# Performance work log

Hardware: AMD Instinct MI355X
Metric: run time of the kernel (lower is better)

Reference implementation:

```python
import jax, jax.numpy as jnp
import numpy as np

D_MODEL = 1024
NUM_HEADS = 16
HEAD_DIM = D_MODEL // NUM_HEADS


def setup_inputs() -> dict:
    key = jax.random.key(0)
    ks = jax.random.split(key, 9)
    B, S = 2, 2048
    s = 1.0 / np.sqrt(D_MODEL)
    return {
        "x": jax.random.normal(ks[0], (B, S, D_MODEL), dtype=jnp.float32),
        "Wq": jax.random.normal(ks[1], (D_MODEL, D_MODEL), dtype=jnp.float32) * s,
        "bq": jnp.zeros((D_MODEL,), dtype=jnp.float32),
        "Wk": jax.random.normal(ks[2], (D_MODEL, D_MODEL), dtype=jnp.float32) * s,
        "bk": jnp.zeros((D_MODEL,), dtype=jnp.float32),
        "Wv": jax.random.normal(ks[3], (D_MODEL, D_MODEL), dtype=jnp.float32) * s,
        "bv": jnp.zeros((D_MODEL,), dtype=jnp.float32),
        "Wo": jax.random.normal(ks[4], (D_MODEL, D_MODEL), dtype=jnp.float32) * s,
        "bo": jnp.zeros((D_MODEL,), dtype=jnp.float32),
    }


def reference(x, Wq, bq, Wk, bk, Wv, bv, Wo, bo):
    B, S, _ = x.shape
    # linear projections then split heads: [B, S, D] -> [B, H, S, hd]
    def split_heads(t):
        return t.reshape(B, S, NUM_HEADS, HEAD_DIM).transpose(0, 2, 1, 3)
    q = split_heads(x @ Wq + bq)
    k = split_heads(x @ Wk + bk)
    v = split_heads(x @ Wv + bv)
    # scores: [B, H, S, S]
    scores = jnp.einsum('bhqd,bhkd->bhqk', q, k) / jnp.sqrt(
        jnp.asarray(HEAD_DIM, dtype=x.dtype))
    attn = jax.nn.softmax(scores, axis=-1)
    # dropout is identity in eval mode
    out = jnp.einsum('bhqk,bhkd->bhqd', attn, v)
    out = out.transpose(0, 2, 1, 3).reshape(B, S, D_MODEL)
    return out @ Wo + bo
```

## Files before the change

### kernel.cpp

```cpp
#include <hip/hip_runtime.h>

#define D_MODEL 1024
#define NHEAD 16
#define HD 64
#define BATCH 2
#define SEQ 2048

typedef unsigned short u16;
typedef unsigned int u32;
typedef __bf16 bf16x8 __attribute__((ext_vector_type(8)));
typedef unsigned short u16x8 __attribute__((ext_vector_type(8)));
typedef short s16x4 __attribute__((ext_vector_type(4)));
typedef float f32x4 __attribute__((ext_vector_type(4)));

#if defined(__has_builtin)
#if __has_builtin(__builtin_amdgcn_exp2f)
#define EXP2(x) __builtin_amdgcn_exp2f(x)
#else
#define EXP2(x) exp2f(x)
#endif
#else
#define EXP2(x) exp2f(x)
#endif

static __device__ __forceinline__ u16 f2bf(float f) {
    union { float f; unsigned u; } v; v.f = f;
    unsigned u = v.u;
    u += 0x7fffu + ((u >> 16) & 1u);
    return (u16)(u >> 16);
}

static __device__ __forceinline__ void gld_lds16(const void* g, void* l) {
    __builtin_amdgcn_global_load_lds(
        (const __attribute__((address_space(1))) void*)g,
        (__attribute__((address_space(3))) void*)l, 16, 0, 0);
}

static __device__ __forceinline__ bf16x8 pack_bf8(f32x4 a, f32x4 b) {
    union { float f; unsigned u; } a0, a1, a2, a3, b0, b1, b2, b3;
    a0.f = a[0]; a1.f = a[1]; a2.f = a[2]; a3.f = a[3];
    b0.f = b[0]; b1.f = b[1]; b2.f = b[2]; b3.f = b[3];
    union { unsigned u[4]; bf16x8 v; } r;
    r.u[0] = __builtin_amdgcn_perm(a1.u, a0.u, 0x07060302u);
    r.u[1] = __builtin_amdgcn_perm(a3.u, a2.u, 0x07060302u);
    r.u[2] = __builtin_amdgcn_perm(b1.u, b0.u, 0x07060302u);
    r.u[3] = __builtin_amdgcn_perm(b3.u, b2.u, 0x07060302u);
    return r.v;
}

__global__ __launch_bounds__(256) void k_convert(const float* __restrict__ x,
                                                 const float* __restrict__ wq,
                                                 const float* __restrict__ wk,
                                                 const float* __restrict__ wv,
                                                 const float* __restrict__ wo,
                                                 u16* __restrict__ xb,
                                                 u16* __restrict__ wt) {
    int z = blockIdx.z;
    if (z == 0) {
        int base = (blockIdx.y * 32 + blockIdx.x) * 256 + threadIdx.x;
#pragma unroll
        for (int p = 0; p < 4; p++) {
            int i = base + p * 262144;
            float4 v = ((const float4*)x)[i];
            ushort4 o = make_ushort4(f2bf(v.x), f2bf(v.y), f2bf(v.z), f2bf(v.w));
            ((ushort4*)xb)[i] = o;
        }
        return;
    }
    __shared__ u16 t[32][33];
    const float* W = z == 1 ? wq : z == 2 ? wk : z == 3 ? wv : wo;
    u16* dst = wt + (size_t)(z - 1) * (D_MODEL * D_MODEL);
    int tx = threadIdx.x & 31, ty = threadIdx.x >> 5;
    int n0 = blockIdx.x * 32, k0 = blockIdx.y * 32;
#pragma unroll
    for (int i = 0; i < 4; i++)
        t[ty + i * 8][tx] = f2bf(W[(size_t)(k0 + ty + i * 8) * D_MODEL + n0 + tx]);
    __syncthreads();
#pragma unroll
    for (int i = 0; i < 4; i++)
        dst[(size_t)(n0 + ty + i * 8) * D_MODEL + k0 + tx] = t[tx][ty + i * 8];
}

__global__ __launch_bounds__(256) void k_gemm(const u16* __restrict__ A,
                                              const u16* __restrict__ WtBase,
                                              const float* __restrict__ b0,
                                              const float* __restrict__ b1,
                                              const float* __restrict__ b2,
                                              u16* __restrict__ oq, u16* __restrict__ ok,
                                              u16* __restrict__ ov) {
    __shared__ u16 lA[2 * 128 * 32];
    __shared__ u16 lB[2 * 128 * 32];
    int tid = threadIdx.x, w = tid >> 6, l = tid & 63, lr = l & 15, lq = l >> 4;
    int z = blockIdx.z;
    const u16* Wt = WtBase + (size_t)z * (D_MODEL * D_MODEL);
    const float* bias = z == 0 ? b0 : z == 1 ? b1 : b2;
    float scale = (z == 0) ? (0.125f * 1.44269504088896340736f) : 1.0f;
    int m0 = blockIdx.y * 128, n0 = blockIdx.x * 128;
    int wm = (w >> 1) * 64, wn = (w & 1) * 64;
    f32x4 acc[4][4];
#pragma unroll
    for (int mi = 0; mi < 4; mi++)
#pragma unroll
        for (int ni = 0; ni < 4; ni++) acc[mi][ni] = (f32x4){0.f, 0.f, 0.f, 0.f};

    int ra = tid >> 2, ca = (tid & 3) * 8;
    const u16* Aba = A + (size_t)(m0 + ra) * D_MODEL + ca;
    const u16* Abb = A + (size_t)(m0 + 64 + ra) * D_MODEL + ca;
    const u16* Bba = Wt + (size_t)(n0 + ra) * D_MODEL + ca;
    const u16* Bbb = Wt + (size_t)(n0 + 64 + ra) * D_MODEL + ca;

    auto stage = [&](int kk, int buf) {
        gld_lds16(Aba + kk, &lA[buf * 4096 + w * 512]);
        gld_lds16(Abb + kk, &lA[buf * 4096 + 2048 + w * 512]);
        gld_lds16(Bba + kk, &lB[buf * 4096 + w * 512]);
        gld_lds16(Bbb + kk, &lB[buf * 4096 + 2048 + w * 512]);
    };

    stage(0, 0);
    __syncthreads();
    int cur = 0;
    for (int t = 0; t < 32; ++t) {
        if (t + 1 < 32) stage((t + 1) * 32, cur ^ 1);
        bf16x8 af[4], bf[4];
#pragma unroll
        for (int mi = 0; mi < 4; mi++)
            af[mi] = *(const bf16x8*)&lA[cur * 4096 + (wm + mi * 16 + lr) * 32 + lq * 8];
#pragma unroll
        for (int ni = 0; ni < 4; ni++)
            bf[ni] = *(const bf16x8*)&lB[cur * 4096 + (wn + ni * 16 + lr) * 32 + lq * 8];
        __builtin_amdgcn_s_setprio(1);
#pragma unroll
        for (int mi = 0; mi < 4; mi++)
#pragma unroll
            for (int ni = 0; ni < 4; ni++)
                acc[mi][ni] = __builtin_amdgcn_mfma_f32_16x16x32_bf16(
                    af[mi], bf[ni], acc[mi][ni], 0, 0, 0);
        __builtin_amdgcn_s_setprio(0);
        __syncthreads();
        cur ^= 1;
    }
#pragma unroll
    for (int mi = 0; mi < 4; mi++) {
#pragma unroll
        for (int ni = 0; ni < 4; ni++) {
            int col = n0 + wn + ni * 16 + lr;
            float bval = bias[col];
            int row0 = m0 + wm + mi * 16 + lq * 4;
            if (z == 2) {
                int b = row0 >> 11, s = row0 & 2047;
                int h = col >> 6, dd = col & 63;
                ushort4 pk;
                pk.x = f2bf(acc[mi][ni][0] + bval);
                pk.y = f2bf(acc[mi][ni][1] + bval);
                pk.z = f2bf(acc[mi][ni][2] + bval);
                pk.w = f2bf(acc[mi][ni][3] + bval);
                *(ushort4*)&ov[((size_t)(b * NHEAD + h) * HD + dd) * SEQ + s] = pk;
            } else {
#pragma unroll
                for (int r = 0; r < 4; r++) {
                    int row = row0 + r;
                    float val = (acc[mi][ni][r] + bval) * scale;
                    u16* op = z == 0 ? oq : ok;
                    int b = row >> 11, s = row & 2047, h = col >> 6, d = col & 63;
                    op[(((size_t)(b * NHEAD + h)) * SEQ + s) * HD + d] = f2bf(val);
                }
            }
        }
    }
}

__global__ __launch_bounds__(256) void k_gout(const u16* __restrict__ A,
                                              const u16* __restrict__ Wt,
                                              const float* __restrict__ bias,
                                              float* __restrict__ outf) {
    __shared__ u16 lA[2 * 64 * 32];
    __shared__ u16 lB[2 * 64 * 32];
    int tid = threadIdx.x, w = tid >> 6, l = tid & 63, lr = l & 15, lq = l >> 4;
    int m0 = blockIdx.y * 64, n0 = blockIdx.x * 64;
    int wm = (w >> 1) * 32, wn = (w & 1) * 32;
    f32x4 acc[2][2];
#pragma unroll
    for (int mi = 0; mi < 2; mi++)
#pragma unroll
        for (int ni = 0; ni < 2; ni++) acc[mi][ni] = (f32x4){0.f, 0.f, 0.f, 0.f};

    int ra = tid >> 2, ca = (tid & 3) * 8;
    const u16* Aba = A + (size_t)(m0 + ra) * D_MODEL + ca;
    const u16* Bba = Wt + (size_t)(n0 + ra) * D_MODEL + ca;

    auto stage = [&](int kk, int buf) {
        gld_lds16(Aba + kk, &lA[buf * 2048 + w * 512]);
        gld_lds16(Bba + kk, &lB[buf * 2048 + w * 512]);
    };

    stage(0, 0);
    __syncthreads();
    int cur = 0;
    for (int t = 0; t < 32; ++t) {
        if (t + 1 < 32) stage((t + 1) * 32, cur ^ 1);
        bf16x8 af[2], bf[2];
#pragma unroll
        for (int mi = 0; mi < 2; mi++)
            af[mi] = *(const bf16x8*)&lA[cur * 2048 + (wm + mi * 16 + lr) * 32 + lq * 8];
#pragma unroll
        for (int ni = 0; ni < 2; ni++)
            bf[ni] = *(const bf16x8*)&lB[cur * 2048 + (wn + ni * 16 + lr) * 32 + lq * 8];
        __builtin_amdgcn_s_setprio(1);
#pragma unroll
        for (int mi = 0; mi < 2; mi++)
#pragma unroll
            for (int ni = 0; ni < 2; ni++)
                acc[mi][ni] = __builtin_amdgcn_mfma_f32_16x16x32_bf16(
                    af[mi], bf[ni], acc[mi][ni], 0, 0, 0);
        __builtin_amdgcn_s_setprio(0);
        __syncthreads();
        cur ^= 1;
    }
#pragma unroll
    for (int mi = 0; mi < 2; mi++)
#pragma unroll
        for (int ni = 0; ni < 2; ni++) {
            int col = n0 + wn + ni * 16 + lr;
            float bval = bias[col];
#pragma unroll
            for (int r = 0; r < 4; r++) {
                int row = m0 + wm + mi * 16 + lq * 4 + r;
                outf[(size_t)row * D_MODEL + col] = acc[mi][ni][r] + bval;
            }
        }
}

static __device__ __forceinline__ int ksw(int row, int col) {
    return row * 64 + ((((col >> 3) ^ (row & 7)) << 3) | (col & 7));
}
static __device__ __forceinline__ int vsw(int row, int col) {
    return row * 128 + ((((col >> 3) ^ (row & 15)) << 3) | (col & 7));
}

__global__ __launch_bounds__(256) void k_attn(const u16* __restrict__ Q,
                                              const u16* __restrict__ K,
                                              const u16* __restrict__ VT,
                                              u16* __restrict__ part0,
                                              u16* __restrict__ part1,
                                              float* __restrict__ lsum, int nsplit) {
    __shared__ __align__(16) u16 lK[128 * 64];
    __shared__ __align__(16) u16 lVt[64 * 128];
    int tid = threadIdx.x, w = tid >> 6, l = tid & 63, lr = l & 15, lq = l >> 4;
    int bl = blockIdx.x;
    int qt = bl / (32 * nsplit);
    int rem = bl - qt * (32 * nsplit);
    int bh = rem / nsplit;
    int ks = rem - bh * nsplit;
    int qb = qt * 128 + w * 32;
    const u16* Qb = Q + (size_t)bh * SEQ * HD;
    const u16* Kb = K + (size_t)bh * SEQ * HD;
    const u16* VTb = VT + (size_t)bh * HD * SEQ;

    bf16x8 qf[2][2];
#pragma unroll
    for (int tq = 0; tq < 2; tq++)
#pragma unroll
        for (int kc = 0; kc < 2; kc++)
            qf[tq][kc] = *(const bf16x8*)&Qb[(size_t)(qb + tq * 16 + lr) * HD +
                                             kc * 32 + lq * 8];
    f32x4 o[2][4];
    f32x4 ol[2];
#pragma unroll
    for (int tq = 0; tq < 2; tq++) {
        ol[tq] = (f32x4){0.f, 0.f, 0.f, 0.f};
#pragma unroll
        for (int di = 0; di < 4; di++) o[tq][di] = (f32x4){0.f, 0.f, 0.f, 0.f};
    }
    union { u16 s[8]; bf16x8 v; } onev;
#pragma unroll
    for (int i = 0; i < 8; i++) onev.s[i] = 0x3F80;
    const bf16x8 vone8 = onev.v;

    int krow = tid >> 3, kch = tid & 7;
    int vrow = tid >> 4, vch = tid & 15;

    int nk = SEQ / nsplit;
    int jbeg = ks * nk, jend = jbeg + nk;

    u16x8 kreg[4], vreg[4];
#pragma unroll
    for (int p = 0; p < 4; p++) {
        kreg[p] = *(const u16x8*)&Kb[(size_t)(jbeg + p * 32 + krow) * HD + kch * 8];
        vreg[p] = *(const u16x8*)&VTb[(size_t)(p * 16 + vrow) * SEQ + jbeg + vch * 8];
    }

    for (int j0 = jbeg; j0 < jend; j0 += 128) {
        __syncthreads();
#pragma unroll
        for (int p = 0; p < 4; p++) {
            *(u16x8*)&lK[ksw(p * 32 + krow, kch * 8)] = kreg[p];
            *(u16x8*)&lVt[vsw(p * 16 + vrow, vch * 8)] = vreg[p];
        }
        __syncthreads();
        if (j0 + 128 < jend) {
            int jn = j0 + 128;
#pragma unroll
            for (int p = 0; p < 4; p++) {
                kreg[p] = *(const u16x8*)&Kb[(size_t)(jn + p * 32 + krow) * HD + kch * 8];
                vreg[p] = *(const u16x8*)&VTb[(size_t)(p * 16 + vrow) * SEQ + jn + vch * 8];
            }
        }

#pragma unroll
        for (int kh = 0; kh < 2; kh++) {
#pragma unroll
            for (int t2 = 0; t2 < 2; t2++) {
                int rA = kh * 64 + t2 * 32 + lr;
                int rB = rA + 16;
                bf16x8 kA0 = *(const bf16x8*)&lK[ksw(rA, lq * 8)];
                bf16x8 kA1 = *(const bf16x8*)&lK[ksw(rA, 32 + lq * 8)];
                bf16x8 kB0 = *(const bf16x8*)&lK[ksw(rB, lq * 8)];
                bf16x8 kB1 = *(const bf16x8*)&lK[ksw(rB, 32 + lq * 8)];
                f32x4 sA0 = (f32x4){0.f, 0.f, 0.f, 0.f};
                f32x4 sA1 = (f32x4){0.f, 0.f, 0.f, 0.f};
                f32x4 sB0 = (f32x4){0.f, 0.f, 0.f, 0.f};
                f32x4 sB1 = (f32x4){0.f, 0.f, 0.f, 0.f};
                __builtin_amdgcn_s_setprio(1);
                sA0 = __builtin_amdgcn_mfma_f32_16x16x32_bf16(kA0, qf[0][0], sA0, 0, 0, 0);
                sB0 = __builtin_amdgcn_mfma_f32_16x16x32_bf16(kB0, qf[0][0], sB0, 0, 0, 0);
                sA1 = __builtin_amdgcn_mfma_f32_16x16x32_bf16(kA0, qf[1][0], sA1, 0, 0, 0);
                sB1 = __builtin_amdgcn_mfma_f32_16x16x32_bf16(kB0, qf[1][0], sB1, 0, 0, 0);
                sA0 = __builtin_amdgcn_mfma_f32_16x16x32_bf16(kA1, qf[0][1], sA0, 0, 0, 0);
                sB0 = __builtin_amdgcn_mfma_f32_16x16x32_bf16(kB1, qf[0][1], sB0, 0, 0, 0);
                sA1 = __builtin_amdgcn_mfma_f32_16x16x32_bf16(kA1, qf[1][1], sA1, 0, 0, 0);
                sB1 = __builtin_amdgcn_mfma_f32_16x16x32_bf16(kB1, qf[1][1], sB1, 0, 0, 0);
                __builtin_amdgcn_s_setprio(0);
#pragma unroll
                for (int r = 0; r < 4; r++) {
                    sA0[r] = EXP2(sA0[r]);
                    sA1[r] = EXP2(sA1[r]);
                    sB0[r] = EXP2(sB0[r]);
                    sB1[r] = EXP2(sB1[r]);
                }
                bf16x8 pf0 = pack_bf8(sA0, sB0);
                bf16x8 pf1 = pack_bf8(sA1, sB1);
                __builtin_amdgcn_s_setprio(1);
                ol[0] = __builtin_amdgcn_mfma_f32_16x16x32_bf16(pf0, vone8, ol[0], 0, 0, 0);
                ol[1] = __builtin_amdgcn_mfma_f32_16x16x32_bf16(pf1, vone8, ol[1], 0, 0, 0);
#pragma unroll
                for (int di = 0; di < 4; di++) {
                    int vr = di * 16 + lr;
                    union { bf16x8 v; s16x4 h[2]; } vv;
                    vv.h[0] = *(const s16x4*)&lVt[vsw(vr, kh * 64 + t2 * 32 + lq * 4)];
                    vv.h[1] = *(const s16x4*)&lVt[vsw(vr, kh * 64 + t2 * 32 + 16 + lq * 4)];
                    o[0][di] = __builtin_amdgcn_mfma_f32_16x16x32_bf16(pf0, vv.v,
                                                                       o[0][di], 0, 0, 0);
                    o[1][di] = __builtin_amdgcn_mfma_f32_16x16x32_bf16(pf1, vv.v,
                                                                       o[1][di], 0, 0, 0);
                }
                __builtin_amdgcn_s_setprio(0);
            }
        }
    }
    int b = bh >> 4, h = bh & 15;
    if (nsplit == 1) {
#pragma unroll
        for (int tq = 0; tq < 2; tq++) {
#pragma unroll
            for (int di = 0; di < 4; di++)
#pragma unroll
                for (int r = 0; r < 4; r++) {
                    int qg = qb + tq * 16 + lq * 4 + r;
                    part0[((size_t)(b * SEQ + qg)) * D_MODEL + h * 64 + di * 16 + lr] =
                        f2bf(o[tq][di][r] / ol[tq][r]);
                }
        }
    } else {
        u16* pdst = (ks == 0) ? part0 : part1;
#pragma unroll
        for (int tq = 0; tq < 2; tq++)
#pragma unroll
            for (int di = 0; di < 4; di++)
#pragma unroll
                for (int r = 0; r < 4; r++) {
                    int qg = qb + tq * 16 + lq * 4 + r;
                    union { _Float16 h; u16 u; } cv;
                    cv.h = (_Float16)o[tq][di][r];
                    pdst[((size_t)(b * SEQ + qg)) * D_MODEL + h * 64 + di * 16 + lr] =
                        cv.u;
                }
        if (lr == 0) {
#pragma unroll
            for (int tq = 0; tq < 2; tq++)
#pragma unroll
                for (int r = 0; r < 4; r++) {
                    int qg = qb + tq * 16 + lq * 4 + r;
                    lsum[(ks * 32 + bh) * 2048 + qg] = ol[tq][r];
                }
        }
    }
}

__global__ __launch_bounds__(256) void k_combine(const u16* __restrict__ p0,
                                                 const u16* __restrict__ p1,
                                                 const float* __restrict__ lsum,
                                                 u16* __restrict__ dst) {
    int i = blockIdx.x * 256 + threadIdx.x;
    size_t a8 = (size_t)i * 8;
    int row = (int)(a8 >> 10);
    int col = (int)(a8 & 1023);
    int b = row >> 11, q = row & 2047, h = col >> 6;
    int mi = ((b << 4) + h) * 2048 + q;
    float inv = 1.0f / (lsum[mi] + lsum[65536 + mi]);
    u16x8 h0 = *(const u16x8*)(p0 + a8);
    u16x8 h1 = *(const u16x8*)(p1 + a8);
    u16x8 out;
#pragma unroll
    for (int j = 0; j < 8; j++) {
        union { _Float16 h; u16 u; } c0, c1;
        c0.u = h0[j]; c1.u = h1[j];
        out[j] = f2bf(((float)c0.h + (float)c1.h) * inv);
    }
    *(u16x8*)(dst + a8) = out;
}

extern "C" void kernel_launch(void* const* d_in, const int* in_sizes, int n_in,
                              void* d_out, int out_size, void* d_ws, size_t ws_size,
                              hipStream_t stream) {
    const float* x  = (const float*)d_in[0];
    const float* Wq = (const float*)d_in[1];
    const float* bq = (const float*)d_in[2];
    const float* Wk = (const float*)d_in[3];
    const float* bk = (const float*)d_in[4];
    const float* Wv = (const float*)d_in[5];
    const float* bv = (const float*)d_in[6];
    const float* Wo = (const float*)d_in[7];
    const float* bo = (const float*)d_in[8];
    float* out = (float*)d_out;

    char* ws = (char*)d_ws;
    u16* xb  = (u16*)ws;
    u16* wt  = (u16*)(ws + (size_t)8 * 1024 * 1024);
    u16* qws = (u16*)(ws + (size_t)16 * 1024 * 1024);
    u16* kws = (u16*)(ws + (size_t)24 * 1024 * 1024);
    u16* vtw = (u16*)(ws + (size_t)32 * 1024 * 1024);
    u16* ao  = (u16*)(ws + (size_t)40 * 1024 * 1024);
    float* ml = (float*)(ws + (size_t)48 * 1024 * 1024);

    int nsplit = (ws_size >= (size_t)49 * 1024 * 1024) ? 2 : 1;
    u16* attn_out = (nsplit == 2) ? xb : ao;

    k_convert<<<dim3(32, 32, 5), 256, 0, stream>>>(x, Wq, Wk, Wv, Wo, xb, wt);
    k_gemm<<<dim3(8, 32, 3), 256, 0, stream>>>(xb, wt, bq, bk, bv, qws, kws, vtw);
    if (nsplit == 2) {
        k_attn<<<16 * 32 * 2, 256, 0, stream>>>(qws, kws, vtw, xb, ao, ml, 2);
        k_combine<<<2048, 256, 0, stream>>>(xb, ao, ml, xb);
    } else {
        k_attn<<<16 * 32, 256, 0, stream>>>(qws, kws, vtw, ao, nullptr, ml, 1);
    }
    k_gout<<<dim3(16, 64), 256, 0, stream>>>(attn_out,
                                             wt + (size_t)3 * D_MODEL * D_MODEL,
                                             bo, out);
}
```

Before: 190.6 us.

## Switch attention inner loop to 32x32x16 MFMA tiles with permuted V layout

Rewrites the attention kernel's QK^T and PV products to use 32x32x16 bf16 MFMA instead of 16x16x32. Each wave now holds a 32-query by 32-key score tile in one f32x16 accumulator. The V projection epilogue permutes sequence positions within 16-element groups so the exp'd score register layout feeds PV directly as an operand. The aim is fewer MFMA issues and fewer LDS reads per key block. In exchange it adds a permuted VT layout that must match exactly, and changes the output write pattern.

```diff
diff --git a/kernel.cpp b/kernel.cpp
--- a/kernel.cpp
+++ b/kernel.cpp
@@ -12,6 +12,7 @@
 typedef unsigned short u16x8 __attribute__((ext_vector_type(8)));
 typedef short s16x4 __attribute__((ext_vector_type(4)));
 typedef float f32x4 __attribute__((ext_vector_type(4)));
+typedef float f32x16 __attribute__((ext_vector_type(16)));
 
 #if defined(__has_builtin)
 #if __has_builtin(__builtin_amdgcn_exp2f)
@@ -149,12 +150,13 @@
             if (z == 2) {
                 int b = row0 >> 11, s = row0 & 2047;
                 int h = col >> 6, dd = col & 63;
+                int sp = (s & ~15) | (((lq & 1) << 3) | ((lq >> 1) << 2));
                 ushort4 pk;
                 pk.x = f2bf(acc[mi][ni][0] + bval);
                 pk.y = f2bf(acc[mi][ni][1] + bval);
                 pk.z = f2bf(acc[mi][ni][2] + bval);
                 pk.w = f2bf(acc[mi][ni][3] + bval);
-                *(ushort4*)&ov[((size_t)(b * NHEAD + h) * HD + dd) * SEQ + s] = pk;
+                *(ushort4*)&ov[((size_t)(b * NHEAD + h) * HD + dd) * SEQ + sp] = pk;
             } else {
 #pragma unroll
                 for (int r = 0; r < 4; r++) {
@@ -245,7 +247,8 @@
                                               float* __restrict__ lsum, int nsplit) {
     __shared__ __align__(16) u16 lK[128 * 64];
     __shared__ __align__(16) u16 lVt[64 * 128];
-    int tid = threadIdx.x, w = tid >> 6, l = tid & 63, lr = l & 15, lq = l >> 4;
+    int tid = threadIdx.x, w = tid >> 6, l = tid & 63;
+    int l31 = l & 31, hi = l >> 5;
     int bl = blockIdx.x;
     int qt = bl / (32 * nsplit);
     int rem = bl - qt * (32 * nsplit);
@@ -256,21 +259,14 @@
     const u16* Kb = K + (size_t)bh * SEQ * HD;
     const u16* VTb = VT + (size_t)bh * HD * SEQ;
 
-    bf16x8 qf[2][2];
-#pragma unroll
-    for (int tq = 0; tq < 2; tq++)
-#pragma unroll
-        for (int kc = 0; kc < 2; kc++)
-            qf[tq][kc] = *(const bf16x8*)&Qb[(size_t)(qb + tq * 16 + lr) * HD +
-                                             kc * 32 + lq * 8];
-    f32x4 o[2][4];
-    f32x4 ol[2];
-#pragma unroll
-    for (int tq = 0; tq < 2; tq++) {
-        ol[tq] = (f32x4){0.f, 0.f, 0.f, 0.f};
-#pragma unroll
-        for (int di = 0; di < 4; di++) o[tq][di] = (f32x4){0.f, 0.f, 0.f, 0.f};
-    }
+    bf16x8 qf[4];
+#pragma unroll
+    for (int m = 0; m < 4; m++)
+        qf[m] = *(const bf16x8*)&Qb[(size_t)(qb + l31) * HD + m * 16 + hi * 8];
+
+    f32x16 o0, o1, ol;
+#pragma unroll
+    for (int r = 0; r < 16; r++) { o0[r] = 0.f; o1[r] = 0.f; ol[r] = 0.f; }
     union { u16 s[8]; bf16x8 v; } onev;
 #pragma unroll
     for (int i = 0; i < 8; i++) onev.s[i] = 0x3F80;
@@ -307,91 +303,67 @@
         }
 
 #pragma unroll
-        for (int kh = 0; kh < 2; kh++) {
-#pragma unroll
-            for (int t2 = 0; t2 < 2; t2++) {
-                int rA = kh * 64 + t2 * 32 + lr;
-                int rB = rA + 16;
-                bf16x8 kA0 = *(const bf16x8*)&lK[ksw(rA, lq * 8)];
-                bf16x8 kA1 = *(const bf16x8*)&lK[ksw(rA, 32 + lq * 8)];
-                bf16x8 kB0 = *(const bf16x8*)&lK[ksw(rB, lq * 8)];
-                bf16x8 kB1 = *(const bf16x8*)&lK[ksw(rB, 32 + lq * 8)];
-                f32x4 sA0 = (f32x4){0.f, 0.f, 0.f, 0.f};
-                f32x4 sA1 = (f32x4){0.f, 0.f, 0.f, 0.f};
-                f32x4 sB0 = (f32x4){0.f, 0.f, 0.f, 0.f};
-                f32x4 sB1 = (f32x4){0.f, 0.f, 0.f, 0.f};
-                __builtin_amdgcn_s_setprio(1);
-                sA0 = __builtin_amdgcn_mfma_f32_16x16x32_bf16(kA0, qf[0][0], sA0, 0, 0, 0);
-                sB0 = __builtin_amdgcn_mfma_f32_16x16x32_bf16(kB0, qf[0][0], sB0, 0, 0, 0);
-                sA1 = __builtin_amdgcn_mfma_f32_16x16x32_bf16(kA0, qf[1][0], sA1, 0, 0, 0);
-                sB1 = __builtin_amdgcn_mfma_f32_16x16x32_bf16(kB0, qf[1][0], sB1, 0, 0, 0);
-                sA0 = __builtin_amdgcn_mfma_f32_16x16x32_bf16(kA1, qf[0][1], sA0, 0, 0, 0);
-                sB0 = __builtin_amdgcn_mfma_f32_16x16x32_bf16(kB1, qf[0][1], sB0, 0, 0, 0);
-                sA1 = __builtin_amdgcn_mfma_f32_16x16x32_bf16(kA1, qf[1][1], sA1, 0, 0, 0);
-                sB1 = __builtin_amdgcn_mfma_f32_16x16x32_bf16(kB1, qf[1][1], sB1, 0, 0, 0);
-                __builtin_amdgcn_s_setprio(0);
-#pragma unroll
-                for (int r = 0; r < 4; r++) {
-                    sA0[r] = EXP2(sA0[r]);
-                    sA1[r] = EXP2(sA1[r]);
-                    sB0[r] = EXP2(sB0[r]);
-                    sB1[r] = EXP2(sB1[r]);
-                }
-                bf16x8 pf0 = pack_bf8(sA0, sB0);
-                bf16x8 pf1 = pack_bf8(sA1, sB1);
-                __builtin_amdgcn_s_setprio(1);
-                ol[0] = __builtin_amdgcn_mfma_f32_16x16x32_bf16(pf0, vone8, ol[0], 0, 0, 0);
-                ol[1] = __builtin_amdgcn_mfma_f32_16x16x32_bf16(pf1, vone8, ol[1], 0, 0, 0);
-#pragma unroll
-                for (int di = 0; di < 4; di++) {
-                    int vr = di * 16 + lr;
-                    union { bf16x8 v; s16x4 h[2]; } vv;
-                    vv.h[0] = *(const s16x4*)&lVt[vsw(vr, kh * 64 + t2 * 32 + lq * 4)];
-                    vv.h[1] = *(const s16x4*)&lVt[vsw(vr, kh * 64 + t2 * 32 + 16 + lq * 4)];
-                    o[0][di] = __builtin_amdgcn_mfma_f32_16x16x32_bf16(pf0, vv.v,
-                                                                       o[0][di], 0, 0, 0);
-                    o[1][di] = __builtin_amdgcn_mfma_f32_16x16x32_bf16(pf1, vv.v,
-                                                                       o[1][di], 0, 0, 0);
-                }
-                __builtin_amdgcn_s_setprio(0);
-            }
+        for (int kb = 0; kb < 128; kb += 32) {
+            bf16x8 kf0 = *(const bf16x8*)&lK[ksw(kb + l31, 0 * 16 + hi * 8)];
+            bf16x8 kf1 = *(const bf16x8*)&lK[ksw(kb + l31, 1 * 16 + hi * 8)];
+            bf16x8 kf2 = *(const bf16x8*)&lK[ksw(kb + l31, 2 * 16 + hi * 8)];
+            bf16x8 kf3 = *(const bf16x8*)&lK[ksw(kb + l31, 3 * 16 + hi * 8)];
+            f32x16 sc;
+#pragma unroll
+            for (int r = 0; r < 16; r++) sc[r] = 0.f;
+            __builtin_amdgcn_s_setprio(1);
+            sc = __builtin_amdgcn_mfma_f32_32x32x16_bf16(kf0, qf[0], sc, 0, 0, 0);
+            sc = __builtin_amdgcn_mfma_f32_32x32x16_bf16(kf1, qf[1], sc, 0, 0, 0);
+            sc = __builtin_amdgcn_mfma_f32_32x32x16_bf16(kf2, qf[2], sc, 0, 0, 0);
+            sc = __builtin_amdgcn_mfma_f32_32x32x16_bf16(kf3, qf[3], sc, 0, 0, 0);
+            __builtin_amdgcn_s_setprio(0);
+#pragma unroll
+            for (int r = 0; r < 16; r++) sc[r] = EXP2(sc[r]);
+            bf16x8 pf0 = pack_bf8((f32x4){sc[0], sc[1], sc[2], sc[3]},
+                                  (f32x4){sc[4], sc[5], sc[6], sc[7]});
+            bf16x8 pf1 = pack_bf8((f32x4){sc[8], sc[9], sc[10], sc[11]},
+                                  (f32x4){sc[12], sc[13], sc[14], sc[15]});
+            bf16x8 v00 = *(const bf16x8*)&lVt[vsw(l31, kb + hi * 8)];
+            bf16x8 v01 = *(const bf16x8*)&lVt[vsw(l31, kb + 16 + hi * 8)];
+            bf16x8 v10 = *(const bf16x8*)&lVt[vsw(32 + l31, kb + hi * 8)];
+            bf16x8 v11 = *(const bf16x8*)&lVt[vsw(32 + l31, kb + 16 + hi * 8)];
+            __builtin_amdgcn_s_setprio(1);
+            ol = __builtin_amdgcn_mfma_f32_32x32x16_bf16(pf0, vone8, ol, 0, 0, 0);
+            ol = __builtin_amdgcn_mfma_f32_32x32x16_bf16(pf1, vone8, ol, 0, 0, 0);
+            o0 = __builtin_amdgcn_mfma_f32_32x32x16_bf16(pf0, v00, o0, 0, 0, 0);
+            o0 = __builtin_amdgcn_mfma_f32_32x32x16_bf16(pf1, v01, o0, 0, 0, 0);
+            o1 = __builtin_amdgcn_mfma_f32_32x32x16_bf16(pf0, v10, o1, 0, 0, 0);
+            o1 = __builtin_amdgcn_mfma_f32_32x32x16_bf16(pf1, v11, o1, 0, 0, 0);
+            __builtin_amdgcn_s_setprio(0);
         }
     }
     int b = bh >> 4, h = bh & 15;
     if (nsplit == 1) {
 #pragma unroll
-        for (int tq = 0; tq < 2; tq++) {
-#pragma unroll
-            for (int di = 0; di < 4; di++)
-#pragma unroll
-                for (int r = 0; r < 4; r++) {
-                    int qg = qb + tq * 16 + lq * 4 + r;
-                    part0[((size_t)(b * SEQ + qg)) * D_MODEL + h * 64 + di * 16 + lr] =
-                        f2bf(o[tq][di][r] / ol[tq][r]);
-                }
+        for (int r = 0; r < 16; r++) {
+            int qg = qb + (r & 3) + 8 * (r >> 2) + 4 * hi;
+            float inv = 1.0f / ol[r];
+            part0[((size_t)(b * SEQ + qg)) * D_MODEL + h * 64 + l31] = f2bf(o0[r] * inv);
+            part0[((size_t)(b * SEQ + qg)) * D_MODEL + h * 64 + 32 + l31] =
+                f2bf(o1[r] * inv);
         }
     } else {
         u16* pdst = (ks == 0) ? part0 : part1;
 #pragma unroll
-        for (int tq = 0; tq < 2; tq++)
-#pragma unroll
-            for (int di = 0; di < 4; di++)
-#pragma unroll
-                for (int r = 0; r < 4; r++) {
-                    int qg = qb + tq * 16 + lq * 4 + r;
-                    union { _Float16 h; u16 u; } cv;
-                    cv.h = (_Float16)o[tq][di][r];
-                    pdst[((size_t)(b * SEQ + qg)) * D_MODEL + h * 64 + di * 16 + lr] =
-                        cv.u;
-                }
-        if (lr == 0) {
-#pragma unroll
-            for (int tq = 0; tq < 2; tq++)
-#pragma unroll
-                for (int r = 0; r < 4; r++) {
-                    int qg = qb + tq * 16 + lq * 4 + r;
-                    lsum[(ks * 32 + bh) * 2048 + qg] = ol[tq][r];
-                }
+        for (int r = 0; r < 16; r++) {
+            int qg = qb + (r & 3) + 8 * (r >> 2) + 4 * hi;
+            union { _Float16 h; u16 u; } c0, c1;
+            c0.h = (_Float16)o0[r];
+            c1.h = (_Float16)o1[r];
+            pdst[((size_t)(b * SEQ + qg)) * D_MODEL + h * 64 + l31] = c0.u;
+            pdst[((size_t)(b * SEQ + qg)) * D_MODEL + h * 64 + 32 + l31] = c1.u;
+        }
+        if (l31 == 0) {
+#pragma unroll
+            for (int r = 0; r < 16; r++) {
+                int qg = qb + (r & 3) + 8 * (r >> 2) + 4 * hi;
+                lsum[(ks * 32 + bh) * 2048 + qg] = ol[r];
+            }
         }
     }
 }
```

Measured after the change: 195.3 us. +2.5%, slower.
